# Performance work log

Hardware: AMD Instinct MI355X
Metric: run time of the kernel (lower is better)

Reference implementation:

```python
import jax, jax.numpy as jnp
import numpy as np

B, T, D_IN, H, K = 8, 1024, 1024, 1024, 3
PAD = (K - 1) // 2


def conv_gates(x, w, b):
    # x: [B,T,C], w: [3H, C, K], b: [3H] -> f,o,z each [B,T,H]
    y = jax.lax.conv_general_dilated(
        x.transpose(0, 2, 1), w, window_strides=(1,), padding=[(PAD, PAD)],
        dimension_numbers=('NCH', 'OIH', 'NCH'))
    g = y.transpose(0, 2, 1) + b  # [B,T,3H]
    f, o, z = jnp.split(g, 3, axis=-1)
    return jax.nn.sigmoid(f), jax.nn.sigmoid(o), jnp.tanh(z)


def fo_pool(f, z):
    # linear recurrence c_t = f_t*c_{t-1} + (1-f_t)*z_t, c_0 = 0; f,z: [B,T,H]
    def step(c, fz):
        ft, zt = fz
        c = ft * c + (1.0 - ft) * zt
        return c, c
    init = jnp.zeros((f.shape[0], f.shape[2]), f.dtype)
    _, cells = jax.lax.scan(step, init, (f.transpose(1, 0, 2), z.transpose(1, 0, 2)))
    return cells.transpose(1, 0, 2)  # [B,T,H]


def qrnn_layer(x, wf, bf, wr, br):
    # forward direction
    f, o, z = conv_gates(x, wf, bf)
    cells = fo_pool(f, z)
    h = cells * o
    # reverse direction: scan from the end (flip, scan, flip back)
    fr, orv, zr = conv_gates(x, wr, br)
    rcells = jnp.flip(fo_pool(jnp.flip(fr, 1), jnp.flip(zr, 1)), 1)
    rh = rcells * orv
    out = jnp.concatenate([h, rh], -1)                      # [B,T,2H]
    last_h = jnp.concatenate([h[:, -1], rh[:, -1]], -1)     # [B,2H]
    last_c = jnp.concatenate([cells[:, -1], rcells[:, -1]], -1)
    return out, last_h, last_c


def setup_inputs() -> dict:
    key = jax.random.key(0)
    ks = jax.random.split(key, 9)
    x = jax.random.normal(ks[0], (B, T, D_IN), jnp.float32)
    lengths = jnp.full((B,), T, dtype=jnp.int64)
    s = 0.02
    # layer 0: in=D_IN, layer 1: in=2H (bidirectional concat)
    w0f = jax.random.normal(ks[1], (3 * H, D_IN, K), jnp.float32) * s
    b0f = jnp.zeros((3 * H,), jnp.float32)
    w0r = jax.random.normal(ks[2], (3 * H, D_IN, K), jnp.float32) * s
    b0r = jnp.zeros((3 * H,), jnp.float32)
    w1f = jax.random.normal(ks[3], (3 * H, 2 * H, K), jnp.float32) * s
    b1f = jnp.zeros((3 * H,), jnp.float32)
    w1r = jax.random.normal(ks[4], (3 * H, 2 * H, K), jnp.float32) * s
    b1r = jnp.zeros((3 * H,), jnp.float32)
    return {"x": x, "lengths": lengths, "w0f": w0f, "b0f": b0f, "w0r": w0r,
            "b0r": b0r, "w1f": w1f, "b1f": b1f, "w1r": w1r, "b1r": b1r}


def reference(x, lengths, w0f, b0f, w0r, b0r, w1f, b1f, w1r, b1r):
    out0, h0, c0 = qrnn_layer(x, w0f, b0f, w0r, b0r)
    out1, h1, c1 = qrnn_layer(out0, w1f, b1f, w1r, b1r)
    # torch: cat along dim 0 then view(num_dir*num_layers, B, H)
    hidden = jnp.concatenate([h0, h1], 0).reshape(4, x.shape[0], H)
    cell = jnp.concatenate([c0, c1], 0).reshape(4, x.shape[0], H)
    return out1, hidden, cell
```

## Files before the change

### kernel.cpp

```cpp
#include <hip/hip_runtime.h>
#include <math.h>

#define BB 8
#define TT 1024
#define HDIM 1024
#define G3 3072
#define NCH 32
#define TC 32
#define TP (TT + 2)

#define SW(r) (((r) >> 1) & 3)

typedef __attribute__((ext_vector_type(8))) short bf16x8;
typedef __attribute__((ext_vector_type(4))) float f32x4;

__device__ __forceinline__ unsigned short f2bf(float f) {
  union { float f; unsigned int u; } c; c.f = f;
  unsigned int u = c.u;
  return (unsigned short)((u + 0x7FFFu + ((u >> 16) & 1u)) >> 16);
}

__device__ __forceinline__ void load_lds16(const void* g, void* l) {
  __builtin_amdgcn_global_load_lds(
      (const __attribute__((address_space(1))) void*)g,
      (__attribute__((address_space(3))) void*)l, 16, 0, 0);
}

__global__ __launch_bounds__(256) void cvt_x_pad_kernel(const float* __restrict__ in,
                                                        unsigned short* __restrict__ out) {
  int b = blockIdx.y;
  int i = (blockIdx.x * 256 + threadIdx.x) * 4;
  int r = i >> 10;
  int c = i & 1023;
  ushort4 o = make_ushort4(0, 0, 0, 0);
  if (r >= 1 && r <= TT) {
    float4 v = *(const float4*)(in + ((size_t)b * TT + (r - 1)) * 1024 + c);
    o.x = f2bf(v.x); o.y = f2bf(v.y); o.z = f2bf(v.z); o.w = f2bf(v.w);
  }
  *(ushort4*)(out + (size_t)b * TP * 1024 + i) = o;
}

__global__ __launch_bounds__(256) void zero_pad_kernel(unsigned short* __restrict__ p) {
  int i = blockIdx.x * 256 + threadIdx.x;
  int b = i >> 12;
  int r = (i >> 11) & 1;
  int c = i & 2047;
  p[((size_t)b * TP + (r ? (TT + 1) : 0)) * 2048 + c] = 0;
}

template<int C>
__global__ __launch_bounds__(256) void cvt_w_kernel(const float* __restrict__ in,
                                                    unsigned short* __restrict__ out) {
  int o = blockIdx.x * 256 + threadIdx.x;
  int c = o & (C - 1);
  int jk = o / C;
  int j = jk % G3;
  int k = jk / G3;
  out[o] = f2bf(in[(size_t)j * (3 * C) + (size_t)c * 3 + k]);
}

template<int C>
__global__ __launch_bounds__(256) void conv_mfma_kernel(
    const unsigned short* __restrict__ x,
    const unsigned short* __restrict__ wt,
    const float* __restrict__ bias,
    float* __restrict__ g)
{
  const int L    = blockIdx.x;
  const int xcd  = L & 7;
  const int sL   = L >> 3;
  const int jt   = xcd * 3 + (sL % 3);
  const int rest = sL / 3;
  const int t0 = (rest & 7) * 128;
  const int j0 = jt * 128;
  const int b  = rest >> 3;

  const int tid  = threadIdx.x;
  const int lane = tid & 63;
  const int wave = tid >> 6;
  const int wm = wave >> 1, wn = wave & 1;

  __shared__ unsigned short As[2][144 * 32];
  __shared__ unsigned short Bs[2][384 * 32];

  f32x4 acc[4][4];
  #pragma unroll
  for (int i = 0; i < 4; i++)
    #pragma unroll
    for (int u = 0; u < 4; u++) acc[i][u] = (f32x4){0.f, 0.f, 0.f, 0.f};

  const unsigned short* xb = x + (size_t)b * TP * C;
  const int srow  = lane >> 2;
  const int sslot = lane & 3;
  const int rq = lane >> 4;
  const int rl = lane & 15;

  auto stage = [&](int sel, int c0) {
    unsigned short* Ab = &As[sel][0];
    unsigned short* Bb = &Bs[sel][0];
    #pragma unroll
    for (int cc = 0; cc < 2; ++cc) {
      int call  = wave * 2 + cc;
      int lrow0 = call << 4;
      int lrow  = lrow0 + srow;
      int q = sslot ^ SW(lrow);
      load_lds16(xb + (size_t)(t0 + lrow) * C + c0 + q * 8, Ab + lrow0 * 32);
    }
    if (wave == 3) {
      int lrow0 = 128;
      int lrow  = lrow0 + srow;
      int q = sslot ^ SW(lrow);
      load_lds16(xb + (size_t)(t0 + lrow) * C + c0 + q * 8, Ab + lrow0 * 32);
    }
    #pragma unroll
    for (int cc = 0; cc < 6; ++cc) {
      int R0 = (wave * 6 + cc) << 4;
      int R  = R0 + srow;
      int k = R >> 7;
      int j = R & 127;
      int q = sslot ^ SW(R);
      load_lds16(wt + (size_t)k * (G3 * C) + (size_t)(j0 + j) * C + c0 + q * 8,
                 Bb + R0 * 32);
    }
  };

  constexpr int NSTEP = C / 32;

  stage(0, 0);

  #pragma unroll 2
  for (int it = 0; it < NSTEP; ++it) {
    const int cur = it & 1;
    if (it + 1 < NSTEP) {
      stage(cur ^ 1, (it + 1) * 32);
      if (wave == 3) asm volatile("s_waitcnt vmcnt(9)" ::: "memory");
      else           asm volatile("s_waitcnt vmcnt(8)" ::: "memory");
    } else {
      asm volatile("s_waitcnt vmcnt(0)" ::: "memory");
    }
    __builtin_amdgcn_s_barrier();
    __builtin_amdgcn_sched_barrier(0);

    const unsigned short* Ac = &As[cur][0];
    const unsigned short* Bc = &Bs[cur][0];
    __builtin_amdgcn_s_setprio(1);
    #pragma unroll
    for (int k = 0; k < 3; ++k) {
      bf16x8 af[4], bfr[4];
      #pragma unroll
      for (int im = 0; im < 4; ++im) {
        int lrow = wm * 64 + im * 16 + rl + k;
        af[im] = *(const bf16x8*)&Ac[lrow * 32 + ((rq ^ SW(lrow)) * 8)];
      }
      #pragma unroll
      for (int in = 0; in < 4; ++in) {
        int R = k * 128 + wn * 64 + in * 16 + rl;
        bfr[in] = *(const bf16x8*)&Bc[R * 32 + ((rq ^ SW(R)) * 8)];
      }
      #pragma unroll
      for (int im = 0; im < 4; ++im)
        #pragma unroll
        for (int in = 0; in < 4; ++in)
          acc[im][in] = __builtin_amdgcn_mfma_f32_16x16x32_bf16(
              af[im], bfr[in], acc[im][in], 0, 0, 0);
    }
    __builtin_amdgcn_s_setprio(0);
    __builtin_amdgcn_s_barrier();
  }

  const bool is_tanh = (j0 >= 2 * HDIM);
  const int row_in_tile = (lane >> 4) * 4;
  float* gb = g + (size_t)b * TT * G3;
  #pragma unroll
  for (int in = 0; in < 4; ++in) {
    int j = j0 + wn * 64 + in * 16 + rl;
    float bv = bias[j];
    #pragma unroll
    for (int im = 0; im < 4; ++im) {
      int tl = wm * 64 + im * 16 + row_in_tile;
      #pragma unroll
      for (int r = 0; r < 4; ++r) {
        float s = acc[im][in][r] + bv;
        float v;
        if (is_tanh) v = 1.f - 2.f / (__expf(2.f * s) + 1.f);
        else         v = 1.f / (1.f + __expf(-s));
        gb[(size_t)(t0 + tl + r) * G3 + j] = v;
      }
    }
  }
}

__global__ __launch_bounds__(256) void pool_chunk_kernel(
    const float* __restrict__ g, float* __restrict__ a_arr,
    float* __restrict__ b_arr, int dir)
{
  int idx = blockIdx.x * 256 + threadIdx.x;
  int h  = idx & (HDIM - 1);
  int b  = (idx >> 10) & (BB - 1);
  int ch = idx >> 13;
  const float* gb = g + (size_t)b * TT * G3 + h;
  float a = 1.f, bacc = 0.f;
  #pragma unroll 8
  for (int s = ch * TC; s < ch * TC + TC; ++s) {
    int t = dir ? (TT - 1 - s) : s;
    size_t go = (size_t)t * G3;
    float f = gb[go];
    float z = gb[go + 2 * HDIM];
    bacc = f * bacc + (1.f - f) * z;
    a *= f;
  }
  a_arr[idx] = a;
  b_arr[idx] = bacc;
}

__global__ __launch_bounds__(256) void pool_scan_kernel(
    const float* __restrict__ a_arr, const float* __restrict__ b_arr,
    float* __restrict__ cinit)
{
  int bh = blockIdx.x * 256 + threadIdx.x;
  float c = 0.f;
  #pragma unroll
  for (int ch = 0; ch < NCH; ++ch) {
    cinit[ch * (BB * HDIM) + bh] = c;
    c = a_arr[ch * (BB * HDIM) + bh] * c + b_arr[ch * (BB * HDIM) + bh];
  }
}

template<int OUT_BF16>
__global__ __launch_bounds__(256) void pool_apply_kernel(
    const float* __restrict__ g, const float* __restrict__ cinit,
    void* __restrict__ out, float* __restrict__ hid, float* __restrict__ cell,
    int dir, int layer)
{
  int idx = blockIdx.x * 256 + threadIdx.x;
  int h  = idx & (HDIM - 1);
  int b  = (idx >> 10) & (BB - 1);
  int ch = idx >> 13;
  const float* gb = g + (size_t)b * TT * G3 + h;
  const int coloff = dir * HDIM;
  float c = cinit[idx];
  #pragma unroll 8
  for (int s = ch * TC; s < ch * TC + TC; ++s) {
    int t = dir ? (TT - 1 - s) : s;
    size_t go = (size_t)t * G3;
    float f = gb[go];
    float o = gb[go + HDIM];
    float z = gb[go + 2 * HDIM];
    c = f * c + (1.f - f) * z;
    float hv = c * o;
    if (OUT_BF16) {
      size_t oo = ((size_t)b * TP + t + 1) * (2 * HDIM) + coloff + h;
      ((unsigned short*)out)[oo] = f2bf(hv);
    } else {
      size_t oo = ((size_t)b * TT + t) * (2 * HDIM) + coloff + h;
      ((float*)out)[oo] = hv;
    }
    if (t == TT - 1) {
      size_t off = (size_t)layer * (BB * 2 * HDIM) + (size_t)b * (2 * HDIM) + coloff + h;
      hid[off] = hv;
      cell[off] = c;
    }
  }
}

extern "C" void kernel_launch(void* const* d_in, const int* in_sizes, int n_in,
                              void* d_out, int out_size, void* d_ws, size_t ws_size,
                              hipStream_t stream) {
  const float* x   = (const float*)d_in[0];
  const float* w0f = (const float*)d_in[2];
  const float* b0f = (const float*)d_in[3];
  const float* w0r = (const float*)d_in[4];
  const float* b0r = (const float*)d_in[5];
  const float* w1f = (const float*)d_in[6];
  const float* b1f = (const float*)d_in[7];
  const float* w1r = (const float*)d_in[8];
  const float* b1r = (const float*)d_in[9];

  float* out1 = (float*)d_out;
  float* hid  = out1 + (size_t)BB * TT * 2 * HDIM;
  float* cell = hid + 4 * BB * HDIM;

  char* ws = (char*)d_ws;
  size_t off = 0;
  float*          g     = (float*)(ws + off);  off += (size_t)BB * TT * G3 * 4;
  unsigned short* out0b = (unsigned short*)(ws + off); off += (size_t)BB * TP * 2 * HDIM * 2;
  unsigned short* xb16  = (unsigned short*)(ws + off); off += (size_t)BB * TP * 1024 * 2;
  unsigned short* wt    = (unsigned short*)(ws + off); off += (size_t)3 * G3 * 2048 * 2;
  float* a_arr = (float*)(ws + off); off += (size_t)NCH * BB * HDIM * 4;
  float* b_arr = (float*)(ws + off); off += (size_t)NCH * BB * HDIM * 4;
  float* cinit = (float*)(ws + off); off += (size_t)NCH * BB * HDIM * 4;

  dim3 blk(256);
  dim3 cgrd(8 * 24 * 8);
  dim3 chgrd(NCH * BB * HDIM / 256);
  dim3 scgrd(BB * HDIM / 256);

  cvt_x_pad_kernel<<<dim3(TP, BB), blk, 0, stream>>>(x, xb16);
  zero_pad_kernel<<<2 * BB * 2048 / 256, blk, 0, stream>>>(out0b);

  #define RUN_POOL(OUTB, outp, dir, layer)                                         \
    pool_chunk_kernel<<<chgrd, blk, 0, stream>>>(g, a_arr, b_arr, dir);            \
    pool_scan_kernel<<<scgrd, blk, 0, stream>>>(a_arr, b_arr, cinit);              \
    pool_apply_kernel<OUTB><<<chgrd, blk, 0, stream>>>(g, cinit, outp, hid, cell,  \
                                                       dir, layer);

  cvt_w_kernel<1024><<<3 * G3 * 1024 / 256, blk, 0, stream>>>(w0f, wt);
  conv_mfma_kernel<1024><<<cgrd, blk, 0, stream>>>(xb16, wt, b0f, g);
  RUN_POOL(1, out0b, 0, 0)

  cvt_w_kernel<1024><<<3 * G3 * 1024 / 256, blk, 0, stream>>>(w0r, wt);
  conv_mfma_kernel<1024><<<cgrd, blk, 0, stream>>>(xb16, wt, b0r, g);
  RUN_POOL(1, out0b, 1, 0)

  cvt_w_kernel<2048><<<3 * G3 * 2048 / 256, blk, 0, stream>>>(w1f, wt);
  conv_mfma_kernel<2048><<<cgrd, blk, 0, stream>>>(out0b, wt, b1f, g);
  RUN_POOL(0, out1, 0, 1)

  cvt_w_kernel<2048><<<3 * G3 * 2048 / 256, blk, 0, stream>>>(w1r, wt);
  conv_mfma_kernel<2048><<<cgrd, blk, 0, stream>>>(out0b, wt, b1r, g);
  RUN_POOL(0, out1, 1, 1)
  #undef RUN_POOL
}
```

Baseline: 1.354 ms.

## Enlarge conv MFMA tile to 256x192 with register double-buffered LDS fragment loads

The conv GEMM block tile grows from 128x128 to 256 time steps by 192 gate columns. Each wave now holds an 8x6 accumulator array, and the grid shrinks to 512 blocks with a new XCD-aware index mapping. Fragment loads from LDS for the next k-tap are interleaved with the MFMAs, and the last pipeline step is peeled out of the loop. Because a tile can now straddle the sigmoid/tanh boundary, the activation is chosen per column. The larger tile cuts global and LDS traffic per flop, but it raises register and LDS pressure to one block per CU and produces fewer blocks than an even wave across CUs would want.

```diff
diff --git a/kernel.cpp b/kernel.cpp
--- a/kernel.cpp
+++ b/kernel.cpp
@@ -60,7 +60,7 @@
 }
 
 template<int C>
-__global__ __launch_bounds__(256) void conv_mfma_kernel(
+__global__ __launch_bounds__(256, 1) void conv_mfma_kernel(
     const unsigned short* __restrict__ x,
     const unsigned short* __restrict__ wt,
     const float* __restrict__ bias,
@@ -69,25 +69,25 @@
   const int L    = blockIdx.x;
   const int xcd  = L & 7;
   const int sL   = L >> 3;
-  const int jt   = xcd * 3 + (sL % 3);
-  const int rest = sL / 3;
-  const int t0 = (rest & 7) * 128;
-  const int j0 = jt * 128;
-  const int b  = rest >> 3;
+  const int jt   = xcd * 2 + (sL & 1);
+  const int rest = sL >> 1;
+  const int t0 = (rest & 3) * 256;
+  const int j0 = jt * 192;
+  const int b  = rest >> 2;
 
   const int tid  = threadIdx.x;
   const int lane = tid & 63;
   const int wave = tid >> 6;
   const int wm = wave >> 1, wn = wave & 1;
 
-  __shared__ unsigned short As[2][144 * 32];
-  __shared__ unsigned short Bs[2][384 * 32];
-
-  f32x4 acc[4][4];
+  __shared__ unsigned short As[2][272 * 32];
+  __shared__ unsigned short Bs[2][576 * 32];
+
+  f32x4 acc[8][6];
   #pragma unroll
-  for (int i = 0; i < 4; i++)
-    #pragma unroll
-    for (int u = 0; u < 4; u++) acc[i][u] = (f32x4){0.f, 0.f, 0.f, 0.f};
+  for (int i = 0; i < 8; i++)
+    #pragma unroll
+    for (int u = 0; u < 6; u++) acc[i][u] = (f32x4){0.f, 0.f, 0.f, 0.f};
 
   const unsigned short* xb = x + (size_t)b * TP * C;
   const int srow  = lane >> 2;
@@ -99,91 +99,101 @@
     unsigned short* Ab = &As[sel][0];
     unsigned short* Bb = &Bs[sel][0];
     #pragma unroll
-    for (int cc = 0; cc < 2; ++cc) {
-      int call  = wave * 2 + cc;
-      int lrow0 = call << 4;
+    for (int cc = 0; cc < 4; ++cc) {
+      int lrow0 = (wave * 4 + cc) << 4;
       int lrow  = lrow0 + srow;
       int q = sslot ^ SW(lrow);
       load_lds16(xb + (size_t)(t0 + lrow) * C + c0 + q * 8, Ab + lrow0 * 32);
     }
     if (wave == 3) {
-      int lrow0 = 128;
+      int lrow0 = 256;
       int lrow  = lrow0 + srow;
       int q = sslot ^ SW(lrow);
       load_lds16(xb + (size_t)(t0 + lrow) * C + c0 + q * 8, Ab + lrow0 * 32);
     }
     #pragma unroll
-    for (int cc = 0; cc < 6; ++cc) {
-      int R0 = (wave * 6 + cc) << 4;
+    for (int cc = 0; cc < 9; ++cc) {
+      int R0 = (wave * 9 + cc) << 4;
       int R  = R0 + srow;
-      int k = R >> 7;
-      int j = R & 127;
-      int q = sslot ^ SW(R);
+      int k  = R / 192;
+      int j  = R - k * 192;
+      int q  = sslot ^ SW(R);
       load_lds16(wt + (size_t)k * (G3 * C) + (size_t)(j0 + j) * C + c0 + q * 8,
                  Bb + R0 * 32);
     }
   };
 
+  auto ldA = [&](const unsigned short* Ac, bf16x8* d, int k) {
+    #pragma unroll
+    for (int im = 0; im < 8; ++im) {
+      int r = wm * 128 + im * 16 + rl + k;
+      d[im] = *(const bf16x8*)&Ac[r * 32 + ((rq ^ SW(r)) * 8)];
+    }
+  };
+  auto ldB = [&](const unsigned short* Bc, bf16x8* d, int k) {
+    #pragma unroll
+    for (int in = 0; in < 6; ++in) {
+      int r = k * 192 + wn * 96 + in * 16 + rl;
+      d[in] = *(const bf16x8*)&Bc[r * 32 + ((rq ^ SW(r)) * 8)];
+    }
+  };
+  auto fm = [&](bf16x8* a, bf16x8* bb) {
+    #pragma unroll
+    for (int im = 0; im < 8; ++im)
+      #pragma unroll
+      for (int in = 0; in < 6; ++in)
+        acc[im][in] = __builtin_amdgcn_mfma_f32_16x16x32_bf16(
+            a[im], bb[in], acc[im][in], 0, 0, 0);
+  };
+  auto compute = [&](int sel) {
+    const unsigned short* Ac = &As[sel][0];
+    const unsigned short* Bc = &Bs[sel][0];
+    bf16x8 a0[8], b0[6], a1[8], b1[6];
+    ldA(Ac, a0, 0); ldB(Bc, b0, 0);
+    ldA(Ac, a1, 1); ldB(Bc, b1, 1);
+    __builtin_amdgcn_s_setprio(1);
+    fm(a0, b0);
+    ldA(Ac, a0, 2); ldB(Bc, b0, 2);
+    fm(a1, b1);
+    fm(a0, b0);
+    __builtin_amdgcn_s_setprio(0);
+  };
+
   constexpr int NSTEP = C / 32;
 
   stage(0, 0);
 
   #pragma unroll 2
-  for (int it = 0; it < NSTEP; ++it) {
+  for (int it = 0; it < NSTEP - 1; ++it) {
     const int cur = it & 1;
-    if (it + 1 < NSTEP) {
-      stage(cur ^ 1, (it + 1) * 32);
-      if (wave == 3) asm volatile("s_waitcnt vmcnt(9)" ::: "memory");
-      else           asm volatile("s_waitcnt vmcnt(8)" ::: "memory");
-    } else {
-      asm volatile("s_waitcnt vmcnt(0)" ::: "memory");
-    }
+    stage(cur ^ 1, (it + 1) * 32);
+    if (wave == 3) asm volatile("s_waitcnt vmcnt(14)" ::: "memory");
+    else           asm volatile("s_waitcnt vmcnt(13)" ::: "memory");
     __builtin_amdgcn_s_barrier();
     __builtin_amdgcn_sched_barrier(0);
-
-    const unsigned short* Ac = &As[cur][0];
-    const unsigned short* Bc = &Bs[cur][0];
-    __builtin_amdgcn_s_setprio(1);
-    #pragma unroll
-    for (int k = 0; k < 3; ++k) {
-      bf16x8 af[4], bfr[4];
-      #pragma unroll
-      for (int im = 0; im < 4; ++im) {
-        int lrow = wm * 64 + im * 16 + rl + k;
-        af[im] = *(const bf16x8*)&Ac[lrow * 32 + ((rq ^ SW(lrow)) * 8)];
-      }
-      #pragma unroll
-      for (int in = 0; in < 4; ++in) {
-        int R = k * 128 + wn * 64 + in * 16 + rl;
-        bfr[in] = *(const bf16x8*)&Bc[R * 32 + ((rq ^ SW(R)) * 8)];
-      }
-      #pragma unroll
-      for (int im = 0; im < 4; ++im)
-        #pragma unroll
-        for (int in = 0; in < 4; ++in)
-          acc[im][in] = __builtin_amdgcn_mfma_f32_16x16x32_bf16(
-              af[im], bfr[in], acc[im][in], 0, 0, 0);
-    }
-    __builtin_amdgcn_s_setprio(0);
+    compute(cur);
     __builtin_amdgcn_s_barrier();
   }
-
-  const bool is_tanh = (j0 >= 2 * HDIM);
+  asm volatile("s_waitcnt vmcnt(0)" ::: "memory");
+  __builtin_amdgcn_s_barrier();
+  __builtin_amdgcn_sched_barrier(0);
+  compute((NSTEP - 1) & 1);
+
   const int row_in_tile = (lane >> 4) * 4;
   float* gb = g + (size_t)b * TT * G3;
   #pragma unroll
-  for (int in = 0; in < 4; ++in) {
-    int j = j0 + wn * 64 + in * 16 + rl;
+  for (int in = 0; in < 6; ++in) {
+    int j = j0 + wn * 96 + in * 16 + rl;
     float bv = bias[j];
-    #pragma unroll
-    for (int im = 0; im < 4; ++im) {
-      int tl = wm * 64 + im * 16 + row_in_tile;
+    const bool is_t = (j >= 2 * HDIM);
+    #pragma unroll
+    for (int im = 0; im < 8; ++im) {
+      int tl = wm * 128 + im * 16 + row_in_tile;
       #pragma unroll
       for (int r = 0; r < 4; ++r) {
         float s = acc[im][in][r] + bv;
-        float v;
-        if (is_tanh) v = 1.f - 2.f / (__expf(2.f * s) + 1.f);
-        else         v = 1.f / (1.f + __expf(-s));
+        float e = __expf(is_t ? 2.f * s : -s);
+        float v = is_t ? (1.f - 2.f / (e + 1.f)) : (1.f / (1.f + e));
         gb[(size_t)(t0 + tl + r) * G3 + j] = v;
       }
     }
@@ -291,7 +301,7 @@
   float* cinit = (float*)(ws + off); off += (size_t)NCH * BB * HDIM * 4;
 
   dim3 blk(256);
-  dim3 cgrd(8 * 24 * 8);
+  dim3 cgrd(512);
   dim3 chgrd(NCH * BB * HDIM / 256);
   dim3 scgrd(BB * HDIM / 256);
 
```

Result: slower. 1.598 ms (+18.0%).
